# Kernel tuning notes

Measured on AMD Instinct MI355X. Metric: run time of the kernel, lower is better.

Reference implementation:

```python
import jax, jax.numpy as jnp
import numpy as np

EMBED_DIM = 1024
NUM_HEADS = 16
HEAD_DIM = EMBED_DIM // NUM_HEADS  # 64


def setup_inputs() -> dict:
    key = jax.random.key(0)
    ks = jax.random.split(key, 9)
    B, S, E, D = 4, 2048, EMBED_DIM, HEAD_DIM
    s_e = 1.0 / np.sqrt(E)
    return {
        "x": jax.random.normal(ks[0], (B, S, E), dtype=jnp.float32),
        "Wq": jax.random.uniform(ks[1], (E, E), jnp.float32, -s_e, s_e),
        "bq": jax.random.uniform(ks[2], (E,), jnp.float32, -s_e, s_e),
        "Wk": jax.random.uniform(ks[3], (E, D), jnp.float32, -s_e, s_e),
        "bk": jax.random.uniform(ks[4], (D,), jnp.float32, -s_e, s_e),
        "Wv": jax.random.uniform(ks[5], (E, D), jnp.float32, -s_e, s_e),
        "bv": jax.random.uniform(ks[6], (D,), jnp.float32, -s_e, s_e),
        "Wo": jax.random.uniform(ks[7], (E, E), jnp.float32, -s_e, s_e),
        "bo": jax.random.uniform(ks[8], (E,), jnp.float32, -s_e, s_e),
    }


def reference(x, Wq, bq, Wk, bk, Wv, bv, Wo, bo):
    B, S, E = x.shape
    H, D = NUM_HEADS, HEAD_DIM
    q = (x @ Wq + bq).reshape(B, S, H, D)           # [B,S,H,D]
    k = x @ Wk + bk                                  # [B,S,D] shared single K head
    v = x @ Wv + bv                                  # [B,S,D] shared single V head
    scale = 1.0 / jnp.sqrt(jnp.asarray(D, x.dtype))
    # broadcast shared K across query heads: [B,H,Sq,Sk]
    scores = jnp.einsum("bqhd,bkd->bhqk", q, k) * scale
    probs = jax.nn.softmax(scores, axis=-1)
    out = jnp.einsum("bhqk,bkd->bqhd", probs, v).reshape(B, S, E)
    return out @ Wo + bo
```

## Files before the change

### kernel.cpp

```cpp
#include <hip/hip_runtime.h>

typedef short  bf16x8 __attribute__((ext_vector_type(8)));
typedef float  f32x4  __attribute__((ext_vector_type(4)));
typedef float  f32x16 __attribute__((ext_vector_type(16)));
typedef unsigned int u32;

__device__ __forceinline__ ushort f2b(float f) {
    union { float f; unsigned u; } c; c.f = f;
    unsigned r = c.u + 0x7fffu + ((c.u >> 16) & 1u);
    return (ushort)(r >> 16);
}

__device__ __forceinline__ unsigned cvtpk(float lo, float hi) {
    unsigned r;
    asm("v_cvt_pk_bf16_f32 %0, %1, %2" : "=v"(r) : "v"(lo), "v"(hi));
    return r;
}

__device__ __forceinline__ float fexp2(float x) {
#if __has_builtin(__builtin_amdgcn_exp2f)
    return __builtin_amdgcn_exp2f(x);
#else
    float r; asm("v_exp_f32 %0, %1" : "=v"(r) : "v"(x)); return r;
#endif
}

__device__ __forceinline__ void gload_lds16(const void* g, void* l) {
    __builtin_amdgcn_global_load_lds(
        (const __attribute__((address_space(1))) u32*)g,
        (__attribute__((address_space(3))) u32*)l, 16, 0, 0);
}

__global__ __launch_bounds__(256) void prep_weights(const float* __restrict__ Wq,
                                                    const float* __restrict__ Wo,
                                                    const float* __restrict__ Wk,
                                                    const float* __restrict__ Wv,
                                                    const float* __restrict__ bq,
                                                    const float* __restrict__ bk,
                                                    const float* __restrict__ bv,
                                                    ushort* __restrict__ WqkvT,
                                                    ushort* __restrict__ WoT,
                                                    float* __restrict__ bqkv) {
    __shared__ float tile[32][33];
    int tx = threadIdx.x, ty = threadIdx.y;
    int z = blockIdx.z;
    const float* in;
    ushort* out;
    int c0, r0 = blockIdx.y * 32;
    const int R = 1024;
    if (z == 0)      { in = Wq; out = WqkvT; c0 = blockIdx.x * 32; }
    else if (z == 1) { in = Wo; out = WoT;   c0 = blockIdx.x * 32; }
    else {
        int x = blockIdx.x;
        if (x == 4) {
            if (blockIdx.y == 0) {
                int i0 = ty * 32 + tx;
                for (int k = i0; k < 1152; k += 256)
                    bqkv[k] = (k < 1024) ? bq[k] : (k < 1088) ? bk[k - 1024] : bv[k - 1088];
            }
            return;
        }
        if (x > 4) return;
        if (x < 2) { in = Wk; out = WqkvT + (size_t)1024 * R; c0 = x * 32; }
        else       { in = Wv; out = WqkvT + (size_t)1088 * R; c0 = (x - 2) * 32; }
    }
    int C = (z == 2) ? 64 : 1024;
#pragma unroll
    for (int i = 0; i < 32; i += 8)
        tile[ty + i][tx] = in[(size_t)(r0 + ty + i) * C + c0 + tx];
    __syncthreads();
#pragma unroll
    for (int i = 0; i < 32; i += 8)
        out[(size_t)(c0 + ty + i) * R + r0 + tx] = f2b(tile[tx][ty + i]);
}

template <bool OUT_BF16, bool FUSE_KV, bool A_F32>
__global__ __launch_bounds__(256, 4) void gemm_bt(const void* __restrict__ Ap,
                                                  const ushort* __restrict__ BT,
                                                  const float* __restrict__ bias,
                                                  void* __restrict__ Y, int M, int N, int K,
                                                  int nq, float scale,
                                                  ushort* __restrict__ Kc,
                                                  ushort* __restrict__ Vc) {
    __shared__ ushort As[64 * 64];
    __shared__ ushort Bs[128 * 64];

    int nwg = gridDim.x * gridDim.y;
    int bid = blockIdx.y * gridDim.x + blockIdx.x;
    int swz = (bid & 7) * (nwg >> 3) + (bid >> 3);
    int bx = swz % gridDim.x, by = swz / gridDim.x;

    int m0 = by * 64, n0 = bx * 128;
    int t = threadIdx.x;
    int lane = t & 63, wid = t >> 6;
    int wr = wid >> 1, wc = wid & 1;
    int fr = lane & 15, fg = lane >> 4;

    int rlane = lane >> 3;
    int scol = (lane & 7) * 8;
    const ushort* asrc = (const ushort*)Ap + (size_t)(m0 + wid * 16 + rlane) * K + scol;
    const float*  afsrc0 = (const float*)Ap + (size_t)(m0 + wid * 16 + rlane) * K + scol;
    const float*  afsrc1 = afsrc0 + (size_t)8 * K;
    const ushort* bsrc = BT + (size_t)(n0 + wid * 32 + rlane) * K + scol;

    f32x4 acc[2][4] = {};

    for (int kb = 0; kb < K; kb += 64) {
        if (A_F32) {
#pragma unroll
            for (int g = 0; g < 2; g++) {
                const float* src = (g ? afsrc1 : afsrc0) + kb;
                float4 v0 = *(const float4*)(src);
                float4 v1 = *(const float4*)(src + 4);
                uint4 pk;
                pk.x = cvtpk(v0.x, v0.y);
                pk.y = cvtpk(v0.z, v0.w);
                pk.z = cvtpk(v1.x, v1.y);
                pk.w = cvtpk(v1.z, v1.w);
                *(uint4*)&As[(wid * 16 + g * 8 + rlane) * 64 + scol] = pk;
            }
        } else {
#pragma unroll
            for (int op = 0; op < 2; op++)
                gload_lds16(asrc + kb + (size_t)op * 8 * K, &As[(wid * 16 + op * 8) * 64]);
        }
#pragma unroll
        for (int op = 0; op < 4; op++)
            gload_lds16(bsrc + kb + (size_t)op * 8 * K, &Bs[(wid * 32 + op * 8) * 64]);
        __syncthreads();
#pragma unroll
        for (int kk = 0; kk < 2; kk++) {
            bf16x8 af[2], bfr[4];
#pragma unroll
            for (int m = 0; m < 2; m++)
                af[m] = *(const bf16x8*)&As[(wr * 32 + m * 16 + fr) * 64 + kk * 32 + fg * 8];
#pragma unroll
            for (int n = 0; n < 4; n++)
                bfr[n] = *(const bf16x8*)&Bs[(wc * 64 + n * 16 + fr) * 64 + kk * 32 + fg * 8];
#pragma unroll
            for (int m = 0; m < 2; m++)
#pragma unroll
                for (int n = 0; n < 4; n++)
                    acc[m][n] = __builtin_amdgcn_mfma_f32_16x16x32_bf16(
                        af[m], bfr[n], acc[m][n], 0, 0, 0);
        }
        __syncthreads();
    }

#pragma unroll
    for (int m = 0; m < 2; m++)
#pragma unroll
        for (int n = 0; n < 4; n++) {
            int col = n0 + wc * 64 + n * 16 + fr;
            float bv = bias[col];
            float sc = (col < nq) ? scale : 1.0f;
            if (FUSE_KV && col >= nq) {
                int dd = col - nq;
                bool isV = dd >= 64;
                dd &= 63;
#pragma unroll
                for (int j = 0; j < 4; j++) {
                    int row = m0 + wr * 32 + m * 16 + fg * 4 + j;
                    int bb = row >> 11, s = row & 2047;
                    ushort hv = f2b(acc[m][n][j] + bv);
                    if (!isV)
                        Kc[((size_t)(bb * 8 + (dd >> 3)) * 2048 + s) * 8 + (dd & 7)] = hv;
                    else {
                        int tt = s >> 6, scn = (s >> 3) & 7, si = s & 7;
                        Vc[(((size_t)(bb * 32 + tt) * 8 + scn) * 64 + dd) * 8 + si] = hv;
                    }
                }
            } else {
#pragma unroll
                for (int j = 0; j < 4; j++) {
                    int row = m0 + wr * 32 + m * 16 + fg * 4 + j;
                    float v = (acc[m][n][j] + bv) * sc;
                    if (OUT_BF16)
                        ((ushort*)Y)[(size_t)row * N + col] = f2b(v);
                    else
                        ((float*)Y)[(size_t)row * N + col] = v;
                }
            }
        }
}

__global__ __launch_bounds__(256, 4) void attn_kernel(const ushort* __restrict__ qkv,
                                                      const ushort* __restrict__ Kc,
                                                      const ushort* __restrict__ Vc,
                                                      ushort* __restrict__ ctx) {
    const int S = 2048, E = 1024, QSTR = 1152;
    __shared__ ushort Kb[2][4096];
    __shared__ ushort Vb[2][4096];

    int b = blockIdx.z, h = blockIdx.y;
    int wid = threadIdx.x >> 6, lane = threadIdx.x & 63;
    int q0 = blockIdx.x * 128 + wid * 32;
    int ql = lane & 31, hi = lane >> 5;

    int c0 = wid * 2, c1 = c0 + 1;
    const ushort* ks0 = Kc + (size_t)(b * 8 + c0) * 2048 * 8 + lane * 8;
    const ushort* ks1 = Kc + (size_t)(b * 8 + c1) * 2048 * 8 + lane * 8;
    const ushort* vs0 = Vc + (size_t)(b * 32 * 8 + c0) * 64 * 8 + lane * 8;
    const ushort* vs1 = Vc + (size_t)(b * 32 * 8 + c1) * 64 * 8 + lane * 8;

    const ushort* qbase = qkv + (size_t)(b * S + q0 + ql) * QSTR + h * 64 + hi * 8;
    bf16x8 qf0 = *(const bf16x8*)(qbase);
    bf16x8 qf1 = *(const bf16x8*)(qbase + 16);
    bf16x8 qf2 = *(const bf16x8*)(qbase + 32);
    bf16x8 qf3 = *(const bf16x8*)(qbase + 48);

    const ushort* kb0 = &Kb[0][hi * 512 + ql * 8];
    const ushort* vb0 = &Vb[0][hi * 512 + ql * 8];

    const bf16x8 ones = {0x3F80, 0x3F80, 0x3F80, 0x3F80, 0x3F80, 0x3F80, 0x3F80, 0x3F80};

    f32x16 acc0 = {}, acc1 = {};
    f32x16 accL = {};

    gload_lds16(ks0, &Kb[0][c0 * 512]);
    gload_lds16(ks1, &Kb[0][c1 * 512]);
    gload_lds16(vs0, &Vb[0][c0 * 512]);
    gload_lds16(vs1, &Vb[0][c1 * 512]);
    __syncthreads();

    int cur = 0;
    for (int t = 0; t < 32; ++t) {
        if (t < 31) {
            int nb = cur ^ 1;
            ks0 += 512; ks1 += 512; vs0 += 4096; vs1 += 4096;
            gload_lds16(ks0, &Kb[nb][c0 * 512]);
            gload_lds16(ks1, &Kb[nb][c1 * 512]);
            gload_lds16(vs0, &Vb[nb][c0 * 512]);
            gload_lds16(vs1, &Vb[nb][c1 * 512]);
        }
        const ushort* kp = kb0 + cur * 4096;
        const ushort* vp = vb0 + cur * 4096;

        f32x16 pt0 = {}, pt1 = {};
#pragma unroll
        for (int s = 0; s < 4; s++) {
            bf16x8 kf0 = *(const bf16x8*)(kp + s * 1024);
            bf16x8 kf1 = *(const bf16x8*)(kp + s * 1024 + 256);
            bf16x8 qs = (s == 0) ? qf0 : (s == 1) ? qf1 : (s == 2) ? qf2 : qf3;
            pt0 = __builtin_amdgcn_mfma_f32_32x32x16_bf16(kf0, qs, pt0, 0, 0, 0);
            pt1 = __builtin_amdgcn_mfma_f32_32x32x16_bf16(kf1, qs, pt1, 0, 0, 0);
        }

#pragma unroll
        for (int r = 0; r < 16; r++) pt0[r] = fexp2(pt0[r]);
#pragma unroll
        for (int r = 0; r < 16; r++) pt1[r] = fexp2(pt1[r]);

#pragma unroll
        for (int ks = 0; ks < 4; ks++) {
            float p0, p1, p2, p3, p4, p5, p6, p7;
            if (ks == 0)      { p0=pt0[0]; p1=pt0[1]; p2=pt0[2]; p3=pt0[3];
                                p4=pt0[4]; p5=pt0[5]; p6=pt0[6]; p7=pt0[7]; }
            else if (ks == 1) { p0=pt0[8]; p1=pt0[9]; p2=pt0[10]; p3=pt0[11];
                                p4=pt0[12]; p5=pt0[13]; p6=pt0[14]; p7=pt0[15]; }
            else if (ks == 2) { p0=pt1[0]; p1=pt1[1]; p2=pt1[2]; p3=pt1[3];
                                p4=pt1[4]; p5=pt1[5]; p6=pt1[6]; p7=pt1[7]; }
            else              { p0=pt1[8]; p1=pt1[9]; p2=pt1[10]; p3=pt1[11];
                                p4=pt1[12]; p5=pt1[13]; p6=pt1[14]; p7=pt1[15]; }
            unsigned w0 = cvtpk(p0, p1);
            unsigned w2 = cvtpk(p4, p5);
            asm volatile("v_permlane32_swap_b32 %0, %1" : "+v"(w0), "+v"(w2));
            unsigned w1 = cvtpk(p2, p3);
            unsigned w3 = cvtpk(p6, p7);
            asm volatile("v_permlane32_swap_b32 %0, %1" : "+v"(w1), "+v"(w3));
            bf16x8 pa;
            ((unsigned*)&pa)[0] = w0;
            ((unsigned*)&pa)[1] = w1;
            ((unsigned*)&pa)[2] = w2;
            ((unsigned*)&pa)[3] = w3;

            bf16x8 va0 = *(const bf16x8*)(vp + ks * 1024);
            bf16x8 va1 = *(const bf16x8*)(vp + ks * 1024 + 256);
            acc0 = __builtin_amdgcn_mfma_f32_32x32x16_bf16(va0, pa, acc0, 0, 0, 0);
            acc1 = __builtin_amdgcn_mfma_f32_32x32x16_bf16(va1, pa, acc1, 0, 0, 0);
            accL = __builtin_amdgcn_mfma_f32_32x32x16_bf16(ones, pa, accL, 0, 0, 0);
        }

        __syncthreads();
        cur ^= 1;
    }

    float inv = 1.f / accL[0];

    ushort* obase = ctx + (size_t)(b * S + q0 + ql) * E + h * 64;
#pragma unroll
    for (int g = 0; g < 4; g++) {
        int d = 8 * g + 4 * hi;
        ushort4 o;
        o.x = f2b(acc0[4 * g + 0] * inv);
        o.y = f2b(acc0[4 * g + 1] * inv);
        o.z = f2b(acc0[4 * g + 2] * inv);
        o.w = f2b(acc0[4 * g + 3] * inv);
        *(ushort4*)(obase + d) = o;
    }
#pragma unroll
    for (int g = 0; g < 4; g++) {
        int d = 32 + 8 * g + 4 * hi;
        ushort4 o;
        o.x = f2b(acc1[4 * g + 0] * inv);
        o.y = f2b(acc1[4 * g + 1] * inv);
        o.z = f2b(acc1[4 * g + 2] * inv);
        o.w = f2b(acc1[4 * g + 3] * inv);
        *(ushort4*)(obase + d) = o;
    }
}

extern "C" void kernel_launch(void* const* d_in, const int* in_sizes, int n_in,
                              void* d_out, int out_size, void* d_ws, size_t ws_size,
                              hipStream_t stream) {
    const int B = 4, S = 2048, E = 1024, D = 64;
    const int M = B * S;
    const int NQKV = 1152;
    const float QSCALE = 0.18033688011112042f;

    const float* x  = (const float*)d_in[0];
    const float* Wq = (const float*)d_in[1];
    const float* bq = (const float*)d_in[2];
    const float* Wk = (const float*)d_in[3];
    const float* bk = (const float*)d_in[4];
    const float* Wv = (const float*)d_in[5];
    const float* bv = (const float*)d_in[6];
    const float* Wo = (const float*)d_in[7];
    const float* bo = (const float*)d_in[8];
    float* out = (float*)d_out;

    char* w = (char*)d_ws;
    ushort* qkv   = (ushort*)w;                w += (size_t)M * NQKV * 2;
    ushort* ctx   = (ushort*)w;                w += (size_t)M * E * 2;
    ushort* WqkvT = (ushort*)w;                w += (size_t)NQKV * E * 2;
    ushort* WoT   = (ushort*)w;                w += (size_t)E * E * 2;
    ushort* Kc    = (ushort*)w;                w += (size_t)B * 8 * S * 8 * 2;
    ushort* Vc    = (ushort*)w;                w += (size_t)B * 32 * 8 * 64 * 8 * 2;
    float*  bqkv  = (float*)w;                 w += 8192;

    prep_weights<<<dim3(32, 32, 3), dim3(32, 8), 0, stream>>>(
        Wq, Wo, Wk, Wv, bq, bk, bv, WqkvT, WoT, bqkv);

    gemm_bt<true, true, true><<<dim3(NQKV / 128, M / 64), 256, 0, stream>>>(
        x, WqkvT, bqkv, qkv, M, NQKV, E, 1024, QSCALE, Kc, Vc);

    attn_kernel<<<dim3(S / 128, 16, B), 256, 0, stream>>>(qkv, Kc, Vc, ctx);

    gemm_bt<false, false, false><<<dim3(E / 128, M / 64), 256, 0, stream>>>(
        ctx, WoT, bo, (void*)out, M, E, E, 0, 1.0f, nullptr, nullptr);
}
```

Measured before the change: 160.6 us.

## Switch GEMM to 32x32x16 MFMA with XOR-swizzled LDS layout

The projection GEMM now computes each warp's 32x64 sub-tile with two 32x32x16 bf16 MFMAs per k-step instead of eight 16x16x32 ones. The A and B tiles are stored in LDS with an XOR swizzle on the 16-byte column slot, which is meant to remove bank conflicts on fragment reads. This cuts the number of LDS reads and MFMA issues per k-block. The epilogue is remapped to the 32x32 accumulator layout, which changes the store pattern and may increase register pressure.

```diff
diff --git a/kernel.cpp b/kernel.cpp
--- a/kernel.cpp
+++ b/kernel.cpp
@@ -82,8 +82,8 @@
                                                   int nq, float scale,
                                                   ushort* __restrict__ Kc,
                                                   ushort* __restrict__ Vc) {
-    __shared__ ushort As[64 * 64];
-    __shared__ ushort Bs[128 * 64];
+    __shared__ alignas(16) ushort As[64 * 64];
+    __shared__ alignas(16) ushort Bs[128 * 64];
 
     int nwg = gridDim.x * gridDim.y;
     int bid = blockIdx.y * gridDim.x + blockIdx.x;
@@ -94,16 +94,17 @@
     int t = threadIdx.x;
     int lane = t & 63, wid = t >> 6;
     int wr = wid >> 1, wc = wid & 1;
-    int fr = lane & 15, fg = lane >> 4;
+    int l31 = lane & 31, hi32 = lane >> 5;
 
     int rlane = lane >> 3;
-    int scol = (lane & 7) * 8;
-    const ushort* asrc = (const ushort*)Ap + (size_t)(m0 + wid * 16 + rlane) * K + scol;
-    const float*  afsrc0 = (const float*)Ap + (size_t)(m0 + wid * 16 + rlane) * K + scol;
+    int cc = lane & 7;
+    int scc = cc ^ (rlane & 7);
+    const ushort* asrc  = (const ushort*)Ap + (size_t)(m0 + wid * 16 + rlane) * K + scc * 8;
+    const float*  afsrc0 = (const float*)Ap + (size_t)(m0 + wid * 16 + rlane) * K + cc * 8;
     const float*  afsrc1 = afsrc0 + (size_t)8 * K;
-    const ushort* bsrc = BT + (size_t)(n0 + wid * 32 + rlane) * K + scol;
-
-    f32x4 acc[2][4] = {};
+    const ushort* bsrc  = BT + (size_t)(n0 + wid * 32 + rlane) * K + scc * 8;
+
+    f32x16 acc[2] = {};
 
     for (int kb = 0; kb < K; kb += 64) {
         if (A_F32) {
@@ -117,7 +118,7 @@
                 pk.y = cvtpk(v0.z, v0.w);
                 pk.z = cvtpk(v1.x, v1.y);
                 pk.w = cvtpk(v1.z, v1.w);
-                *(uint4*)&As[(wid * 16 + g * 8 + rlane) * 64 + scol] = pk;
+                *(uint4*)&As[(wid * 16 + g * 8 + rlane) * 64 + scc * 8] = pk;
             }
         } else {
 #pragma unroll
@@ -128,60 +129,55 @@
         for (int op = 0; op < 4; op++)
             gload_lds16(bsrc + kb + (size_t)op * 8 * K, &Bs[(wid * 32 + op * 8) * 64]);
         __syncthreads();
-#pragma unroll
-        for (int kk = 0; kk < 2; kk++) {
-            bf16x8 af[2], bfr[4];
-#pragma unroll
-            for (int m = 0; m < 2; m++)
-                af[m] = *(const bf16x8*)&As[(wr * 32 + m * 16 + fr) * 64 + kk * 32 + fg * 8];
-#pragma unroll
-            for (int n = 0; n < 4; n++)
-                bfr[n] = *(const bf16x8*)&Bs[(wc * 64 + n * 16 + fr) * 64 + kk * 32 + fg * 8];
-#pragma unroll
-            for (int m = 0; m < 2; m++)
-#pragma unroll
-                for (int n = 0; n < 4; n++)
-                    acc[m][n] = __builtin_amdgcn_mfma_f32_16x16x32_bf16(
-                        af[m], bfr[n], acc[m][n], 0, 0, 0);
+
+        int arow = wr * 32 + l31;
+        int brow0 = wc * 64 + l31, brow1 = brow0 + 32;
+        int rx = l31 & 7;
+#pragma unroll
+        for (int s = 0; s < 4; s++) {
+            int slot = (2 * s + hi32) ^ rx;
+            bf16x8 af  = *(const bf16x8*)&As[arow * 64 + slot * 8];
+            bf16x8 bf0 = *(const bf16x8*)&Bs[brow0 * 64 + slot * 8];
+            bf16x8 bf1 = *(const bf16x8*)&Bs[brow1 * 64 + slot * 8];
+            acc[0] = __builtin_amdgcn_mfma_f32_32x32x16_bf16(af, bf0, acc[0], 0, 0, 0);
+            acc[1] = __builtin_amdgcn_mfma_f32_32x32x16_bf16(af, bf1, acc[1], 0, 0, 0);
         }
         __syncthreads();
     }
 
 #pragma unroll
-    for (int m = 0; m < 2; m++)
-#pragma unroll
-        for (int n = 0; n < 4; n++) {
-            int col = n0 + wc * 64 + n * 16 + fr;
-            float bv = bias[col];
-            float sc = (col < nq) ? scale : 1.0f;
-            if (FUSE_KV && col >= nq) {
-                int dd = col - nq;
-                bool isV = dd >= 64;
-                dd &= 63;
-#pragma unroll
-                for (int j = 0; j < 4; j++) {
-                    int row = m0 + wr * 32 + m * 16 + fg * 4 + j;
-                    int bb = row >> 11, s = row & 2047;
-                    ushort hv = f2b(acc[m][n][j] + bv);
-                    if (!isV)
-                        Kc[((size_t)(bb * 8 + (dd >> 3)) * 2048 + s) * 8 + (dd & 7)] = hv;
-                    else {
-                        int tt = s >> 6, scn = (s >> 3) & 7, si = s & 7;
-                        Vc[(((size_t)(bb * 32 + tt) * 8 + scn) * 64 + dd) * 8 + si] = hv;
-                    }
-                }
-            } else {
-#pragma unroll
-                for (int j = 0; j < 4; j++) {
-                    int row = m0 + wr * 32 + m * 16 + fg * 4 + j;
-                    float v = (acc[m][n][j] + bv) * sc;
-                    if (OUT_BF16)
-                        ((ushort*)Y)[(size_t)row * N + col] = f2b(v);
-                    else
-                        ((float*)Y)[(size_t)row * N + col] = v;
+    for (int n = 0; n < 2; n++) {
+        int col = n0 + wc * 64 + n * 32 + l31;
+        float bv = bias[col];
+        float sc = (col < nq) ? scale : 1.0f;
+        if (FUSE_KV && col >= nq) {
+            int dd = col - nq;
+            bool isV = dd >= 64;
+            dd &= 63;
+#pragma unroll
+            for (int r = 0; r < 16; r++) {
+                int row = m0 + wr * 32 + (r & 3) + 8 * (r >> 2) + 4 * hi32;
+                int bb = row >> 11, s = row & 2047;
+                ushort hv = f2b(acc[n][r] + bv);
+                if (!isV)
+                    Kc[((size_t)(bb * 8 + (dd >> 3)) * 2048 + s) * 8 + (dd & 7)] = hv;
+                else {
+                    int tt = s >> 6, scn = (s >> 3) & 7, si = s & 7;
+                    Vc[(((size_t)(bb * 32 + tt) * 8 + scn) * 64 + dd) * 8 + si] = hv;
                 }
             }
-        }
+        } else {
+#pragma unroll
+            for (int r = 0; r < 16; r++) {
+                int row = m0 + wr * 32 + (r & 3) + 8 * (r >> 2) + 4 * hi32;
+                float v = (acc[n][r] + bv) * sc;
+                if (OUT_BF16)
+                    ((ushort*)Y)[(size_t)row * N + col] = f2b(v);
+                else
+                    ((float*)Y)[(size_t)row * N + col] = v;
+            }
+        }
+    }
 }
 
 __global__ __launch_bounds__(256, 4) void attn_kernel(const ushort* __restrict__ qkv,
```

New measurement: 151.3 us. 1.06x faster.
